# Optimization experiments

Hardware: AMD Instinct MI355X
Metric: run time of the kernel (lower is better)

The kernel has to match this reference:

```python
import jax, jax.numpy as jnp
import numpy as np

N, K = 200000, 32


def setup_inputs() -> dict:
    key = jax.random.key(0)
    k1, k2, k3, k4, k5 = jax.random.split(key, 5)
    V = jax.random.normal(k1, (N, 3), dtype=jnp.float32)
    V_def = jax.random.normal(k2, (N, 3), dtype=jnp.float32)
    nbrs = jax.random.randint(k3, (N, K), 0, N)
    wgts = jax.random.uniform(k4, (N, K), dtype=jnp.float32)
    pad = jax.random.uniform(k5, (N, K)) < 0.3
    wgts = jnp.where(pad, 0.0, wgts)
    return {"V": V, "V_def": V_def, "nbrs": nbrs, "wgts": wgts}


def reference(V, V_def, nbrs, wgts):
    mask = jax.lax.stop_gradient((wgts != 0).astype(V.dtype))  # [N,K]
    edges = V[nbrs] - V[:, None]                                # [N,K,3] base edges
    mesh_hood = jnp.swapaxes(edges * mask[..., None], 1, 2)     # [N,3,K]
    tru_hood = jnp.swapaxes(edges * wgts[..., None], 1, 2)      # [N,3,K] weighted base edges
    rot_hood = jnp.swapaxes(V_def[nbrs] - V_def[:, None], 1, 2) # [N,3,K] deformed edges
    # per-vertex 3x3 covariance: sum_k rot_hood[:,i,k] * tru_hood[:,j,k]
    tmp = jnp.einsum('nik,njk->nij', rot_hood, tru_hood)        # [N,3,3]
    U, s, Vh = jnp.linalg.svd(tmp, full_matrices=False)
    Vt = jnp.swapaxes(Vh, 1, 2)  # torch.svd-style V matrix (named Vt in source)
    # R = (Vt @ U^T)^T = U @ Vt^T
    R = jnp.einsum('nij,nkj->nik', U, jnp.swapaxes(Vt, 1, 2))
    dets = jnp.linalg.det(R)                                    # [N]
    last_row = Vt[:, -1, :] * dets[:, None]                     # flip last row by det sign
    Vt = jnp.concatenate([Vt[:, :-1], last_row[:, None]], axis=1)
    R = jnp.einsum('nij,nkj->nik', U, jnp.swapaxes(Vt, 1, 2))   # proper rotation, det=+1
    R_tru = jnp.einsum('nij,njk->nik', R, mesh_hood)            # [N,3,K]
    diff = rot_hood - R_tru
    arap = jnp.sum(diff * diff, axis=1) * wgts * mask           # [N,K]
    return jnp.mean(jnp.sum(arap, axis=-1))
```

## Files before the change

### kernel.cpp

```cpp
#include <hip/hip_runtime.h>
#include <hip/hip_bf16.h>

#define NV   200000
#define KN   32
#define TPB  256
#define NSLICE 4
#define SLICEW 50000

#define F_EPS  5.9604645e-8f
#define F_UNFL 1.1754944e-38f
#define F_TOL  (10.0f * F_EPS)

__device__ __forceinline__ float fdiv_(float a, float b) { return __fdividef(a, b); }
__device__ __forceinline__ float fsqrt_(float x) { return __builtin_amdgcn_sqrtf(x); }

__global__ __launch_bounds__(256) void pack_kernel(const float* __restrict__ V,
                                                   const float* __restrict__ Vd,
                                                   float* __restrict__ wsf) {
    int i = blockIdx.x * 256 + threadIdx.x;
    if (i < NV * 3) {
        int n = i / 3;
        int c = i - n * 3;
        wsf[(size_t)n * 8 + c]     = V[i];
        wsf[(size_t)n * 8 + 3 + c] = Vd[i];
    }
}

__device__ __forceinline__ void slartg_(float f, float g, float& c, float& s, float& r) {
    if (g == 0.0f)      { c = 1.0f; s = 0.0f; r = f; }
    else if (f == 0.0f) { c = 0.0f; s = copysignf(1.0f, g); r = fabsf(g); }
    else {
        float d = fsqrt_(f * f + g * g);
        c = fdiv_(fabsf(f), d);
        r = copysignf(d, f);
        s = fdiv_(g, r);
    }
}

__device__ __forceinline__ void slas2_(float f, float g, float h, float& ssmin, float& ssmax) {
    float fa = fabsf(f), ga = fabsf(g), ha = fabsf(h);
    float fhmn = fminf(fa, ha), fhmx = fmaxf(fa, ha);
    if (fhmn == 0.0f) {
        ssmin = 0.0f;
        if (fhmx == 0.0f) ssmax = ga;
        else {
            float mx = fmaxf(fhmx, ga), mn = fminf(fhmx, ga);
            float q = fdiv_(mn, mx);
            ssmax = mx * fsqrt_(1.0f + q * q);
        }
    } else {
        if (ga < fhmx) {
            float as_ = 1.0f + fdiv_(fhmn, fhmx);
            float at  = fdiv_(fhmx - fhmn, fhmx);
            float au  = fdiv_(ga, fhmx); au = au * au;
            float c   = fdiv_(2.0f, fsqrt_(as_ * as_ + au) + fsqrt_(at * at + au));
            ssmin = fhmn * c;
            ssmax = fdiv_(fhmx, c);
        } else {
            float au = fdiv_(fhmx, ga);
            if (au == 0.0f) { ssmin = fdiv_(fhmn * fhmx, ga); ssmax = ga; }
            else {
                float as_ = 1.0f + fdiv_(fhmn, fhmx);
                float at  = fdiv_(fhmx - fhmn, fhmx);
                float t1 = as_ * au, t2 = at * au;
                float c = fdiv_(1.0f, fsqrt_(1.0f + t1 * t1) + fsqrt_(1.0f + t2 * t2));
                ssmin = (fhmn * c) * au;
                ssmin = ssmin + ssmin;
                ssmax = fdiv_(ga, c + c);
            }
        }
    }
}

__device__ void slasv2_(float f, float g, float h,
                        float& ssmin, float& ssmax,
                        float& snr, float& csr, float& snl, float& csl) {
    float ft = f, fa = fabsf(f), ht = h, ha = fabsf(h);
    int pmax = 1;
    bool swp = (ha > fa);
    if (swp) {
        pmax = 3;
        float t = ft; ft = ht; ht = t;
        t = fa; fa = ha; ha = t;
    }
    float gt = g, ga = fabsf(g);
    float clt = 0.f, crt = 0.f, slt = 0.f, srt = 0.f;
    if (ga == 0.0f) {
        ssmin = ha; ssmax = fa;
        clt = 1.0f; crt = 1.0f; slt = 0.0f; srt = 0.0f;
    } else {
        bool gasmal = true;
        if (ga > fa) {
            pmax = 2;
            if (fdiv_(fa, ga) < F_EPS) {
                gasmal = false;
                ssmax = ga;
                ssmin = (ha > 1.0f) ? fdiv_(fa, fdiv_(ga, ha)) : (fdiv_(fa, ga) * ha);
                clt = 1.0f; slt = fdiv_(ht, gt); srt = 1.0f; crt = fdiv_(ft, gt);
            }
        }
        if (gasmal) {
            float dd = fa - ha;
            float l_ = (dd == fa) ? 1.0f : fdiv_(dd, fa);
            float m_ = fdiv_(gt, ft);
            float t_ = 2.0f - l_;
            float mm = m_ * m_, tt = t_ * t_;
            float s_ = fsqrt_(tt + mm);
            float r_ = (l_ == 0.0f) ? fabsf(m_) : fsqrt_(l_ * l_ + mm);
            float a_ = 0.5f * (s_ + r_);
            ssmin = fdiv_(ha, a_);
            ssmax = fa * a_;
            float tv;
            if (mm == 0.0f) {
                if (l_ == 0.0f) tv = copysignf(2.0f, ft) * copysignf(1.0f, gt);
                else            tv = fdiv_(gt, copysignf(dd, ft)) + fdiv_(m_, t_);
            } else {
                tv = (fdiv_(m_, s_ + t_) + fdiv_(m_, r_ + l_)) * (1.0f + a_);
            }
            float l2 = fsqrt_(tv * tv + 4.0f);
            crt = fdiv_(2.0f, l2);
            srt = fdiv_(tv, l2);
            clt = fdiv_(crt + srt * m_, a_);
            slt = fdiv_(ht, ft) * fdiv_(srt, a_);
        }
    }
    if (swp) { csl = srt; snl = crt; csr = slt; snr = clt; }
    else     { csl = clt; snl = slt; csr = crt; snr = srt; }
    float tsign = 1.0f;
    if (pmax == 1) tsign = copysignf(1.0f, csr) * copysignf(1.0f, csl) * copysignf(1.0f, f);
    if (pmax == 2) tsign = copysignf(1.0f, snr) * copysignf(1.0f, csl) * copysignf(1.0f, g);
    if (pmax == 3) tsign = copysignf(1.0f, snr) * copysignf(1.0f, snl) * copysignf(1.0f, h);
    ssmax = copysignf(ssmax, tsign);
    ssmin = copysignf(ssmin, tsign * copysignf(1.0f, f) * copysignf(1.0f, h));
}

template<int RA, int RB>
__device__ __forceinline__ void rot_rows(float A[3][3], float c, float s) {
    #pragma unroll
    for (int j = 0; j < 3; ++j) {
        float x = A[RA][j], y = A[RB][j];
        A[RA][j] = c * x + s * y;
        A[RB][j] = c * y - s * x;
    }
}
template<int CA, int CB>
__device__ __forceinline__ void rot_cols(float A[3][3], float c, float s) {
    #pragma unroll
    for (int i = 0; i < 3; ++i) {
        float x = A[i][CA], y = A[i][CB];
        A[i][CA] = c * x + s * y;
        A[i][CB] = c * y - s * x;
    }
}
template<int RA, int RB>
__device__ __forceinline__ void swap_rows(float A[3][3]) {
    #pragma unroll
    for (int j = 0; j < 3; ++j) { float t = A[RA][j]; A[RA][j] = A[RB][j]; A[RB][j] = t; }
}
template<int CA, int CB>
__device__ __forceinline__ void swap_cols(float A[3][3]) {
    #pragma unroll
    for (int i = 0; i < 3; ++i) { float t = A[i][CA]; A[i][CA] = A[i][CB]; A[i][CB] = t; }
}

__device__ void bdsqr3(float d[3], float e[2], float U[3][3], float VT[3][3]) {
    float thresh;
    {
        float sminoa = fabsf(d[0]);
        if (sminoa != 0.0f) {
            float mu = sminoa;
            mu = fabsf(d[1]) * fdiv_(mu, mu + fabsf(e[0]));
            sminoa = fminf(sminoa, mu);
            if (sminoa != 0.0f) {
                mu = fabsf(d[2]) * fdiv_(mu, mu + fabsf(e[1]));
                sminoa = fminf(sminoa, mu);
            }
        }
        sminoa = sminoa * 0.57735026919f;
        thresh = fmaxf(F_TOL * sminoa, 54.0f * F_UNFL);
    }

    const bool mir = fabsf(d[0]) < fabsf(d[2]);
    if (mir) {
        float t = d[0]; d[0] = d[2]; d[2] = t;
        t = e[0]; e[0] = e[1]; e[1] = t;
        float Un[3][3], Vn[3][3];
        #pragma unroll
        for (int i = 0; i < 3; ++i)
            #pragma unroll
            for (int j = 0; j < 3; ++j) { Un[i][j] = VT[2 - j][i]; Vn[i][j] = U[j][2 - i]; }
        #pragma unroll
        for (int i = 0; i < 3; ++i)
            #pragma unroll
            for (int j = 0; j < 3; ++j) { U[i][j] = Un[i][j]; VT[i][j] = Vn[i][j]; }
    }

    int iter = 0;
    bool tail22 = false;
    bool aborted = false;

    for (;;) {
        if (iter > 54) { aborted = true; break; }
        if (fabsf(e[1]) <= thresh) { e[1] = 0.0f; tail22 = true; break; }
        float smax = fmaxf(fabsf(d[2]), fmaxf(fabsf(e[1]), fabsf(d[1])));
        if (fabsf(e[0]) <= thresh) {
            e[0] = 0.0f;
            float sigmn, sigmx, sinr, cosr, sinl, cosl;
            slasv2_(d[1], e[1], d[2], sigmn, sigmx, sinr, cosr, sinl, cosl);
            d[1] = sigmx; d[2] = sigmn; e[1] = 0.0f;
            rot_rows<1, 2>(VT, cosr, sinr); rot_cols<1, 2>(U, cosl, sinl);
            break;
        }
        smax = fmaxf(smax, fmaxf(fabsf(e[0]), fabsf(d[0])));
        float sminl = 0.0f;
        bool conv = false;
        {
            if (fabsf(e[1]) <= F_TOL * fabsf(d[2])) { e[1] = 0.0f; continue; }
            float mu = fabsf(d[0]); sminl = mu;
            if (fabsf(e[0]) <= F_TOL * mu) { e[0] = 0.0f; conv = true; }
            else {
                mu = fabsf(d[1]) * fdiv_(mu, mu + fabsf(e[0]));
                sminl = fminf(sminl, mu);
                if (fabsf(e[1]) <= F_TOL * mu) { e[1] = 0.0f; conv = true; }
                else {
                    mu = fabsf(d[2]) * fdiv_(mu, mu + fabsf(e[1]));
                    sminl = fminf(sminl, mu);
                }
            }
        }
        if (conv) continue;
        float shift = 0.0f, rdum;
        if (3.0f * F_TOL * fdiv_(sminl, smax) <= fmaxf(F_EPS, 0.01f * F_TOL)) {
            shift = 0.0f;
        } else {
            float sll = fabsf(d[0]);
            slas2_(d[1], e[1], d[2], shift, rdum);
            if (sll > 0.0f) { float q = fdiv_(shift, sll); if (q * q < F_EPS) shift = 0.0f; }
        }
        iter += 2;
        if (shift == 0.0f) {
            float cs = 1.0f, oldcs = 1.0f, sn, oldsn, r;
            float c1, s1, oc1, os1, c2, s2, oc2, os2;
            slartg_(d[0] * cs, e[0], cs, sn, r);
            slartg_(oldcs * r, d[1] * sn, oldcs, oldsn, d[0]);
            c1 = cs; s1 = sn; oc1 = oldcs; os1 = oldsn;
            slartg_(d[1] * cs, e[1], cs, sn, r);
            e[0] = oldsn * r;
            slartg_(oldcs * r, d[2] * sn, oldcs, oldsn, d[1]);
            c2 = cs; s2 = sn; oc2 = oldcs; os2 = oldsn;
            float h = d[2] * cs; d[2] = h * oldcs; e[1] = h * oldsn;
            rot_rows<0, 1>(VT, c1, s1);  rot_rows<1, 2>(VT, c2, s2);
            rot_cols<0, 1>(U, oc1, os1); rot_cols<1, 2>(U, oc2, os2);
            if (fabsf(e[1]) <= thresh) e[1] = 0.0f;
        } else {
            float f = (fabsf(d[0]) - shift) * (copysignf(1.0f, d[0]) + fdiv_(shift, d[0]));
            float g = e[0], cosr, sinr, cosl, sinl, r;
            float cr1, sr1, cl1, sl1, cr2, sr2, cl2, sl2;
            slartg_(f, g, cosr, sinr, r);
            f = cosr * d[0] + sinr * e[0];
            e[0] = cosr * e[0] - sinr * d[0];
            g = sinr * d[1];
            d[1] = cosr * d[1];
            slartg_(f, g, cosl, sinl, r);
            d[0] = r;
            f = cosl * e[0] + sinl * d[1];
            d[1] = cosl * d[1] - sinl * e[0];
            g = sinl * e[1];
            e[1] = cosl * e[1];
            cr1 = cosr; sr1 = sinr; cl1 = cosl; sl1 = sinl;
            slartg_(f, g, cosr, sinr, r);
            e[0] = r;
            f = cosr * d[1] + sinr * e[1];
            e[1] = cosr * e[1] - sinr * d[1];
            g = sinr * d[2];
            d[2] = cosr * d[2];
            slartg_(f, g, cosl, sinl, r);
            d[1] = r;
            f = cosl * e[1] + sinl * d[2];
            d[2] = cosl * d[2] - sinl * e[1];
            cr2 = cosr; sr2 = sinr; cl2 = cosl; sl2 = sinl;
            e[1] = f;
            rot_rows<0, 1>(VT, cr1, sr1); rot_rows<1, 2>(VT, cr2, sr2);
            rot_cols<0, 1>(U, cl1, sl1);  rot_cols<1, 2>(U, cl2, sl2);
            if (fabsf(e[1]) <= thresh) e[1] = 0.0f;
        }
    }
    if (tail22 && !aborted) {
        if (fabsf(e[0]) <= thresh) {
            e[0] = 0.0f;
        } else {
            float sigmn, sigmx, sinr, cosr, sinl, cosl;
            slasv2_(d[0], e[0], d[1], sigmn, sigmx, sinr, cosr, sinl, cosl);
            d[0] = sigmx; d[1] = sigmn; e[0] = 0.0f;
            rot_rows<0, 1>(VT, cosr, sinr); rot_cols<0, 1>(U, cosl, sinl);
        }
    }
    if (mir) {
        float Un[3][3], Vn[3][3];
        #pragma unroll
        for (int i = 0; i < 3; ++i)
            #pragma unroll
            for (int j = 0; j < 3; ++j) { Un[i][j] = VT[j][i]; Vn[i][j] = U[j][i]; }
        #pragma unroll
        for (int i = 0; i < 3; ++i)
            #pragma unroll
            for (int j = 0; j < 3; ++j) { U[i][j] = Un[i][j]; VT[i][j] = Vn[i][j]; }
    }
    #pragma unroll
    for (int i = 0; i < 3; ++i) {
        if (d[i] < 0.0f) {
            d[i] = -d[i];
            VT[i][0] = -VT[i][0]; VT[i][1] = -VT[i][1]; VT[i][2] = -VT[i][2];
        }
    }
    {
        int isub = 1; float smin = d[0];
        if (d[1] <= smin) { isub = 2; smin = d[1]; }
        if (d[2] <= smin) { isub = 3; smin = d[2]; }
        if (isub != 3) {
            if (isub == 1) { d[0] = d[2]; d[2] = smin; swap_rows<0, 2>(VT); swap_cols<0, 2>(U); }
            else           { d[1] = d[2]; d[2] = smin; swap_rows<1, 2>(VT); swap_cols<1, 2>(U); }
        }
    }
    {
        int isub = 1; float smin = d[0];
        if (d[1] <= smin) { isub = 2; smin = d[1]; }
        if (isub != 2) { d[0] = d[1]; d[1] = smin; swap_rows<0, 1>(VT); swap_cols<0, 1>(U); }
    }
}

__device__ float svd_energy(const float T[3][3], float Srr, float See) {
    float A[3][3];
    #pragma unroll
    for (int i = 0; i < 3; ++i) { A[i][0] = T[i][0]; A[i][1] = T[i][1]; A[i][2] = T[i][2]; }

    float d[3], e[2];
    float tq0, v1, v2;
    float tp0, u2;
    float tq1, v22;
    {
        float a00 = A[0][0], a10 = A[1][0], a20 = A[2][0];
        float xn = fsqrt_(a10 * a10 + a20 * a20);
        if (xn == 0.0f) { tq0 = 0.0f; v1 = 0.0f; v2 = 0.0f; d[0] = a00; }
        else {
            float beta = -copysignf(fsqrt_(a00 * a00 + xn * xn), a00);
            tq0 = fdiv_(beta - a00, beta);
            float inv = fdiv_(1.0f, a00 - beta);
            v1 = a10 * inv; v2 = a20 * inv;
            d[0] = beta;
        }
        #pragma unroll
        for (int j = 1; j < 3; ++j) {
            float w = A[0][j] + v1 * A[1][j] + v2 * A[2][j];
            w *= tq0;
            A[0][j] -= w; A[1][j] -= w * v1; A[2][j] -= w * v2;
        }
    }
    {
        float a01 = A[0][1], a02 = A[0][2];
        float xn = fabsf(a02);
        if (xn == 0.0f) { tp0 = 0.0f; u2 = 0.0f; e[0] = a01; }
        else {
            float beta = -copysignf(fsqrt_(a01 * a01 + a02 * a02), a01);
            tp0 = fdiv_(beta - a01, beta);
            u2 = fdiv_(a02, a01 - beta);
            e[0] = beta;
        }
        #pragma unroll
        for (int i = 1; i < 3; ++i) {
            float w = A[i][1] + u2 * A[i][2];
            w *= tp0;
            A[i][1] -= w; A[i][2] -= w * u2;
        }
    }
    {
        float a11 = A[1][1], a21 = A[2][1];
        float xn = fabsf(a21);
        if (xn == 0.0f) { tq1 = 0.0f; v22 = 0.0f; d[1] = a11; }
        else {
            float beta = -copysignf(fsqrt_(a11 * a11 + a21 * a21), a11);
            tq1 = fdiv_(beta - a11, beta);
            v22 = fdiv_(a21, a11 - beta);
            d[1] = beta;
        }
        float w = A[1][2] + v22 * A[2][2];
        w *= tq1;
        A[1][2] -= w; A[2][2] -= w * v22;
        e[1] = A[1][2];
        d[2] = A[2][2];
    }

    float U[3][3], VT[3][3];
    {
        float h11 = 1.0f - tq1;
        float h12 = -tq1 * v22;
        float h22 = 1.0f - tq1 * v22 * v22;
        float w0 = 1.0f;
        float w1 = v1 * h11 + v2 * h12;
        float w2 = v1 * h12 + v2 * h22;
        U[0][0] = 1.0f - tq0 * w0;  U[0][1] = -tq0 * w1;           U[0][2] = -tq0 * w2;
        U[1][0] = -tq0 * v1 * w0;   U[1][1] = h11 - tq0 * v1 * w1; U[1][2] = h12 - tq0 * v1 * w2;
        U[2][0] = -tq0 * v2 * w0;   U[2][1] = h12 - tq0 * v2 * w1; U[2][2] = h22 - tq0 * v2 * w2;
        VT[0][0] = 1.0f; VT[0][1] = 0.0f;               VT[0][2] = 0.0f;
        VT[1][0] = 0.0f; VT[1][1] = 1.0f - tp0;         VT[1][2] = -tp0 * u2;
        VT[2][0] = 0.0f; VT[2][1] = -tp0 * u2;          VT[2][2] = 1.0f - tp0 * u2 * u2;
    }

    bdsqr3(d, e, U, VT);

    float detU = U[0][0] * (U[1][1] * U[2][2] - U[1][2] * U[2][1])
               - U[0][1] * (U[1][0] * U[2][2] - U[1][2] * U[2][0])
               + U[0][2] * (U[1][0] * U[2][1] - U[1][1] * U[2][0]);
    float detV = VT[0][0] * (VT[1][1] * VT[2][2] - VT[1][2] * VT[2][1])
               - VT[0][1] * (VT[1][0] * VT[2][2] - VT[1][2] * VT[2][0])
               + VT[0][2] * (VT[1][0] * VT[2][1] - VT[1][1] * VT[2][0]);
    float det = detU * detV;

    float cross = 0.0f;
    #pragma unroll
    for (int k = 0; k < 3; ++k) {
        float w0 = VT[k][0], w1 = VT[k][1], w2 = det * VT[k][2];
        #pragma unroll
        for (int i = 0; i < 3; ++i) {
            float Rik = U[i][0] * w0 + U[i][1] * w1 + U[i][2] * w2;
            cross += T[i][k] * Rik;
        }
    }
    return Srr + See - 2.0f * cross;
}

__global__ __launch_bounds__(TPB, 4) void gather_kernel(
    const float4* __restrict__ P,
    const int*    __restrict__ nbrs, const float* __restrict__ wgts,
    float4* __restrict__ Tout)
{
    const int t = blockIdx.x * TPB + threadIdx.x;
    const int v = t >> 2;
    const int p = t & 3;
    if (v >= NV) return;

    float4 a0 = P[(size_t)v * 2];
    float2 b0 = ((const float2*)P)[(size_t)v * 4 + 2];
    const float vx = a0.x, vy = a0.y, vz = a0.z;
    const float dx = a0.w, dy = b0.x, dz = b0.y;

    const int4*   nb4 = (const int4*)  (nbrs + (size_t)v * KN) + p * 2;
    const float4* w4  = (const float4*)(wgts + (size_t)v * KN) + p * 2;
    int4   n0 = nb4[0], n1 = nb4[1];
    float4 q0 = w4[0],  q1 = w4[1];
    const int   ids[8] = { n0.x, n0.y, n0.z, n0.w, n1.x, n1.y, n1.z, n1.w };
    const float wss[8] = { q0.x, q0.y, q0.z, q0.w, q1.x, q1.y, q1.z, q1.w };

    float T00 = 0, T01 = 0, T02 = 0, T10 = 0, T11 = 0, T12 = 0, T20 = 0, T21 = 0, T22 = 0;
    float Srr = 0, See = 0;

    #pragma unroll
    for (int sl = 0; sl < NSLICE; ++sl) {
        const int lo = sl * SLICEW;
        const int hi = lo + SLICEW;
        #pragma unroll
        for (int k = 0; k < 8; ++k) {
            int nb = ids[k];
            if (nb >= lo && nb < hi) {
                float w  = wss[k];
                float4 a = P[(size_t)nb * 2];
                float2 b = ((const float2*)P)[(size_t)nb * 4 + 2];
                float e0 = a.x - vx, e1 = a.y - vy, e2 = a.z - vz;
                float r0 = a.w - dx, r1 = b.x - dy, r2 = b.y - dz;
                float we0 = w * e0, we1 = w * e1, we2 = w * e2;
                T00 += r0 * we0; T01 += r0 * we1; T02 += r0 * we2;
                T10 += r1 * we0; T11 += r1 * we1; T12 += r1 * we2;
                T20 += r2 * we0; T21 += r2 * we1; T22 += r2 * we2;
                Srr += w * (r0 * r0 + r1 * r1 + r2 * r2);
                See += we0 * e0 + we1 * e1 + we2 * e2;
            }
        }
    }

    #define RED4(x) x += __shfl_xor(x, 1); x += __shfl_xor(x, 2);
    RED4(T00) RED4(T01) RED4(T02) RED4(T10) RED4(T11) RED4(T12)
    RED4(T20) RED4(T21) RED4(T22) RED4(Srr) RED4(See)
    #undef RED4

    if (p == 0) Tout[(size_t)v * 3 + 0] = make_float4(T00, T01, T02, T10);
    if (p == 1) Tout[(size_t)v * 3 + 1] = make_float4(T11, T12, T20, T21);
    if (p == 2) Tout[(size_t)v * 3 + 2] = make_float4(T22, Srr, See, 0.0f);
}

__global__ __launch_bounds__(TPB) void svd_kernel(
    const float4* __restrict__ Tin, float* __restrict__ out)
{
    __shared__ float s_red[TPB / 64];
    const int tid = threadIdx.x;
    const int n   = blockIdx.x * TPB + tid;
    float E = 0.0f;
    if (n < NV) {
        float4 q0 = Tin[(size_t)n * 3 + 0];
        float4 q1 = Tin[(size_t)n * 3 + 1];
        float4 q2 = Tin[(size_t)n * 3 + 2];
        float T[3][3] = {{q0.x, q0.y, q0.z}, {q0.w, q1.x, q1.y}, {q1.z, q1.w, q2.x}};
        E = svd_energy(T, q2.y, q2.z);
    }
    #pragma unroll
    for (int off = 32; off > 0; off >>= 1) E += __shfl_down(E, off);
    if ((tid & 63) == 0) s_red[tid >> 6] = E;
    __syncthreads();
    if (tid == 0) {
        float t = 0.0f;
        #pragma unroll
        for (int i = 0; i < TPB / 64; ++i) t += s_red[i];
        atomicAdd(out, t * (1.0f / (float)NV));
    }
}

template<bool PACKED>
__global__ __launch_bounds__(TPB) void arap_fused(
    const float*  __restrict__ Vr, const float* __restrict__ Vdr,
    const float4* __restrict__ P,
    const int*    __restrict__ nbrs, const float* __restrict__ wgts,
    float* __restrict__ out)
{
    __shared__ float s_red[TPB / 64];
    const int tid = threadIdx.x;
    const int n   = blockIdx.x * TPB + tid;
    float E = 0.0f;
    if (n < NV) {
        float vx, vy, vz, dx, dy, dz;
        if (PACKED) {
            float4 a0 = P[(size_t)n * 2];
            float2 b0 = ((const float2*)P)[(size_t)n * 4 + 2];
            vx = a0.x; vy = a0.y; vz = a0.z; dx = a0.w; dy = b0.x; dz = b0.y;
        } else {
            vx = Vr [3 * n]; vy = Vr [3 * n + 1]; vz = Vr [3 * n + 2];
            dx = Vdr[3 * n]; dy = Vdr[3 * n + 1]; dz = Vdr[3 * n + 2];
        }
        float T[3][3] = {{0, 0, 0}, {0, 0, 0}, {0, 0, 0}};
        float Srr = 0.0f, See = 0.0f;
        for (int k = 0; k < KN; ++k) {
            int   nb = nbrs[(size_t)n * KN + k];
            float w  = wgts[(size_t)n * KN + k];
            float e0, e1, e2, r0, r1, r2;
            if (PACKED) {
                float4 a = P[(size_t)nb * 2];
                float2 b = ((const float2*)P)[(size_t)nb * 4 + 2];
                e0 = a.x - vx; e1 = a.y - vy; e2 = a.z - vz;
                r0 = a.w - dx; r1 = b.x - dy; r2 = b.y - dz;
            } else {
                e0 = Vr [3 * nb] - vx; e1 = Vr [3 * nb + 1] - vy; e2 = Vr [3 * nb + 2] - vz;
                r0 = Vdr[3 * nb] - dx; r1 = Vdr[3 * nb + 1] - dy; r2 = Vdr[3 * nb + 2] - dz;
            }
            float we0 = w * e0, we1 = w * e1, we2 = w * e2;
            T[0][0] += r0 * we0; T[0][1] += r0 * we1; T[0][2] += r0 * we2;
            T[1][0] += r1 * we0; T[1][1] += r1 * we1; T[1][2] += r1 * we2;
            T[2][0] += r2 * we0; T[2][1] += r2 * we1; T[2][2] += r2 * we2;
            Srr += w * (r0 * r0 + r1 * r1 + r2 * r2);
            See += we0 * e0 + we1 * e1 + we2 * e2;
        }
        E = svd_energy(T, Srr, See);
    }
    #pragma unroll
    for (int off = 32; off > 0; off >>= 1) E += __shfl_down(E, off);
    if ((tid & 63) == 0) s_red[tid >> 6] = E;
    __syncthreads();
    if (tid == 0) {
        float t = 0.0f;
        #pragma unroll
        for (int i = 0; i < TPB / 64; ++i) t += s_red[i];
        atomicAdd(out, t * (1.0f / (float)NV));
    }
}

extern "C" void kernel_launch(void* const* d_in, const int* in_sizes, int n_in,
                              void* d_out, int out_size, void* d_ws, size_t ws_size,
                              hipStream_t stream) {
    (void)in_sizes; (void)n_in; (void)out_size;
    const float* V  = (const float*)d_in[0];
    const float* Vd = (const float*)d_in[1];
    const int*   nb = (const int*)  d_in[2];
    const float* wg = (const float*)d_in[3];
    float* out = (float*)d_out;

    hipMemsetAsync(out, 0, sizeof(float), stream);

    const size_t tab_bytes  = (size_t)NV * 32;
    const size_t tmat_bytes = (size_t)NV * 48;
    const int pblk = (NV * 3 + 255) / 256;

    if (ws_size >= tab_bytes + tmat_bytes) {
        float*  wsf  = (float*)d_ws;
        float4* tout = (float4*)((char*)d_ws + tab_bytes);
        pack_kernel<<<pblk, 256, 0, stream>>>(V, Vd, wsf);
        const int gblk = (NV * 4 + TPB - 1) / TPB;
        gather_kernel<<<gblk, TPB, 0, stream>>>((const float4*)wsf, nb, wg, tout);
        const int sblk = (NV + TPB - 1) / TPB;
        svd_kernel<<<sblk, TPB, 0, stream>>>((const float4*)tout, out);
    } else if (ws_size >= tab_bytes) {
        float* wsf = (float*)d_ws;
        pack_kernel<<<pblk, 256, 0, stream>>>(V, Vd, wsf);
        const int nblk = (NV + TPB - 1) / TPB;
        arap_fused<true><<<nblk, TPB, 0, stream>>>(nullptr, nullptr,
            (const float4*)wsf, nb, wg, out);
    } else {
        const int nblk = (NV + TPB - 1) / TPB;
        arap_fused<false><<<nblk, TPB, 0, stream>>>(V, Vd, nullptr, nb, wg, out);
    }
}
```

Before: 95.45 us.

## Fuse gather and SVD kernels via shared memory staging of covariance

Merges the neighbor-gather kernel and the per-vertex SVD kernel into one kernel. Four threads per vertex accumulate the covariance, the 11 values are staged in shared memory, and then one wavefront of 64 threads runs the SVD energy and does an atomic add per block. This removes the global write and read of the 48-byte-per-vertex covariance buffer and one kernel launch. In exchange only a quarter of each block's threads do the SVD phase, which may leave the ALUs underused, and there are more atomics, one per 64 vertices. The grid assumes NV is divisible by 64.

```diff
diff --git a/kernel.cpp b/kernel.cpp
--- a/kernel.cpp
+++ b/kernel.cpp
@@ -4,6 +4,7 @@
 #define NV   200000
 #define KN   32
 #define TPB  256
+#define VPB  64
 #define NSLICE 4
 #define SLICEW 50000
 
@@ -429,87 +430,76 @@
     return Srr + See - 2.0f * cross;
 }
 
-__global__ __launch_bounds__(TPB, 4) void gather_kernel(
+__global__ __launch_bounds__(TPB, 4) void arap_kernel(
     const float4* __restrict__ P,
     const int*    __restrict__ nbrs, const float* __restrict__ wgts,
-    float4* __restrict__ Tout)
+    float* __restrict__ out)
 {
-    const int t = blockIdx.x * TPB + threadIdx.x;
-    const int v = t >> 2;
-    const int p = t & 3;
-    if (v >= NV) return;
-
-    float4 a0 = P[(size_t)v * 2];
-    float2 b0 = ((const float2*)P)[(size_t)v * 4 + 2];
-    const float vx = a0.x, vy = a0.y, vz = a0.z;
-    const float dx = a0.w, dy = b0.x, dz = b0.y;
-
-    const int4*   nb4 = (const int4*)  (nbrs + (size_t)v * KN) + p * 2;
-    const float4* w4  = (const float4*)(wgts + (size_t)v * KN) + p * 2;
-    int4   n0 = nb4[0], n1 = nb4[1];
-    float4 q0 = w4[0],  q1 = w4[1];
-    const int   ids[8] = { n0.x, n0.y, n0.z, n0.w, n1.x, n1.y, n1.z, n1.w };
-    const float wss[8] = { q0.x, q0.y, q0.z, q0.w, q1.x, q1.y, q1.z, q1.w };
-
-    float T00 = 0, T01 = 0, T02 = 0, T10 = 0, T11 = 0, T12 = 0, T20 = 0, T21 = 0, T22 = 0;
-    float Srr = 0, See = 0;
-
-    #pragma unroll
-    for (int sl = 0; sl < NSLICE; ++sl) {
-        const int lo = sl * SLICEW;
-        const int hi = lo + SLICEW;
-        #pragma unroll
-        for (int k = 0; k < 8; ++k) {
-            int nb = ids[k];
-            if (nb >= lo && nb < hi) {
-                float w  = wss[k];
-                float4 a = P[(size_t)nb * 2];
-                float2 b = ((const float2*)P)[(size_t)nb * 4 + 2];
-                float e0 = a.x - vx, e1 = a.y - vy, e2 = a.z - vz;
-                float r0 = a.w - dx, r1 = b.x - dy, r2 = b.y - dz;
-                float we0 = w * e0, we1 = w * e1, we2 = w * e2;
-                T00 += r0 * we0; T01 += r0 * we1; T02 += r0 * we2;
-                T10 += r1 * we0; T11 += r1 * we1; T12 += r1 * we2;
-                T20 += r2 * we0; T21 += r2 * we1; T22 += r2 * we2;
-                Srr += w * (r0 * r0 + r1 * r1 + r2 * r2);
-                See += we0 * e0 + we1 * e1 + we2 * e2;
-            }
-        }
-    }
-
-    #define RED4(x) x += __shfl_xor(x, 1); x += __shfl_xor(x, 2);
-    RED4(T00) RED4(T01) RED4(T02) RED4(T10) RED4(T11) RED4(T12)
-    RED4(T20) RED4(T21) RED4(T22) RED4(Srr) RED4(See)
-    #undef RED4
-
-    if (p == 0) Tout[(size_t)v * 3 + 0] = make_float4(T00, T01, T02, T10);
-    if (p == 1) Tout[(size_t)v * 3 + 1] = make_float4(T11, T12, T20, T21);
-    if (p == 2) Tout[(size_t)v * 3 + 2] = make_float4(T22, Srr, See, 0.0f);
-}
-
-__global__ __launch_bounds__(TPB) void svd_kernel(
-    const float4* __restrict__ Tin, float* __restrict__ out)
-{
-    __shared__ float s_red[TPB / 64];
+    __shared__ float sT[VPB][13];
+
     const int tid = threadIdx.x;
-    const int n   = blockIdx.x * TPB + tid;
-    float E = 0.0f;
-    if (n < NV) {
-        float4 q0 = Tin[(size_t)n * 3 + 0];
-        float4 q1 = Tin[(size_t)n * 3 + 1];
-        float4 q2 = Tin[(size_t)n * 3 + 2];
-        float T[3][3] = {{q0.x, q0.y, q0.z}, {q0.w, q1.x, q1.y}, {q1.z, q1.w, q2.x}};
-        E = svd_energy(T, q2.y, q2.z);
-    }
-    #pragma unroll
-    for (int off = 32; off > 0; off >>= 1) E += __shfl_down(E, off);
-    if ((tid & 63) == 0) s_red[tid >> 6] = E;
+    const int g   = tid >> 2;
+    const int p   = tid & 3;
+    const int v   = blockIdx.x * VPB + g;
+
+    {
+        float4 a0 = P[(size_t)v * 2];
+        float2 b0 = ((const float2*)P)[(size_t)v * 4 + 2];
+        const float vx = a0.x, vy = a0.y, vz = a0.z;
+        const float dx = a0.w, dy = b0.x, dz = b0.y;
+
+        const int4*   nb4 = (const int4*)  (nbrs + (size_t)v * KN) + p * 2;
+        const float4* w4  = (const float4*)(wgts + (size_t)v * KN) + p * 2;
+        int4   n0 = nb4[0], n1 = nb4[1];
+        float4 q0 = w4[0],  q1 = w4[1];
+        const int   ids[8] = { n0.x, n0.y, n0.z, n0.w, n1.x, n1.y, n1.z, n1.w };
+        const float wss[8] = { q0.x, q0.y, q0.z, q0.w, q1.x, q1.y, q1.z, q1.w };
+
+        float T00 = 0, T01 = 0, T02 = 0, T10 = 0, T11 = 0, T12 = 0, T20 = 0, T21 = 0, T22 = 0;
+        float Srr = 0, See = 0;
+
+        #pragma unroll
+        for (int sl = 0; sl < NSLICE; ++sl) {
+            const int lo = sl * SLICEW;
+            const int hi = lo + SLICEW;
+            #pragma unroll
+            for (int k = 0; k < 8; ++k) {
+                int nb = ids[k];
+                if (nb >= lo && nb < hi) {
+                    float w  = wss[k];
+                    float4 a = P[(size_t)nb * 2];
+                    float2 b = ((const float2*)P)[(size_t)nb * 4 + 2];
+                    float e0 = a.x - vx, e1 = a.y - vy, e2 = a.z - vz;
+                    float r0 = a.w - dx, r1 = b.x - dy, r2 = b.y - dz;
+                    float we0 = w * e0, we1 = w * e1, we2 = w * e2;
+                    T00 += r0 * we0; T01 += r0 * we1; T02 += r0 * we2;
+                    T10 += r1 * we0; T11 += r1 * we1; T12 += r1 * we2;
+                    T20 += r2 * we0; T21 += r2 * we1; T22 += r2 * we2;
+                    Srr += w * (r0 * r0 + r1 * r1 + r2 * r2);
+                    See += we0 * e0 + we1 * e1 + we2 * e2;
+                }
+            }
+        }
+
+        #define RED4(x) x += __shfl_xor(x, 1); x += __shfl_xor(x, 2);
+        RED4(T00) RED4(T01) RED4(T02) RED4(T10) RED4(T11) RED4(T12)
+        RED4(T20) RED4(T21) RED4(T22) RED4(Srr) RED4(See)
+        #undef RED4
+
+        if (p == 0) { sT[g][0] = T00; sT[g][1] = T01; sT[g][2]  = T02; sT[g][3] = T10; }
+        if (p == 1) { sT[g][4] = T11; sT[g][5] = T12; sT[g][6]  = T20; sT[g][7] = T21; }
+        if (p == 2) { sT[g][8] = T22; sT[g][9] = Srr; sT[g][10] = See; }
+    }
     __syncthreads();
-    if (tid == 0) {
-        float t = 0.0f;
-        #pragma unroll
-        for (int i = 0; i < TPB / 64; ++i) t += s_red[i];
-        atomicAdd(out, t * (1.0f / (float)NV));
+
+    if (tid < VPB) {
+        float T[3][3] = {{sT[tid][0], sT[tid][1], sT[tid][2]},
+                         {sT[tid][3], sT[tid][4], sT[tid][5]},
+                         {sT[tid][6], sT[tid][7], sT[tid][8]}};
+        float E = svd_energy(T, sT[tid][9], sT[tid][10]);
+        #pragma unroll
+        for (int off = 32; off > 0; off >>= 1) E += __shfl_down(E, off);
+        if (tid == 0) atomicAdd(out, E * (1.0f / (float)NV));
     }
 }
 
@@ -582,24 +572,14 @@
 
     hipMemsetAsync(out, 0, sizeof(float), stream);
 
-    const size_t tab_bytes  = (size_t)NV * 32;
-    const size_t tmat_bytes = (size_t)NV * 48;
+    const size_t tab_bytes = (size_t)NV * 32;
     const int pblk = (NV * 3 + 255) / 256;
 
-    if (ws_size >= tab_bytes + tmat_bytes) {
-        float*  wsf  = (float*)d_ws;
-        float4* tout = (float4*)((char*)d_ws + tab_bytes);
-        pack_kernel<<<pblk, 256, 0, stream>>>(V, Vd, wsf);
-        const int gblk = (NV * 4 + TPB - 1) / TPB;
-        gather_kernel<<<gblk, TPB, 0, stream>>>((const float4*)wsf, nb, wg, tout);
-        const int sblk = (NV + TPB - 1) / TPB;
-        svd_kernel<<<sblk, TPB, 0, stream>>>((const float4*)tout, out);
-    } else if (ws_size >= tab_bytes) {
+    if (ws_size >= tab_bytes) {
         float* wsf = (float*)d_ws;
         pack_kernel<<<pblk, 256, 0, stream>>>(V, Vd, wsf);
-        const int nblk = (NV + TPB - 1) / TPB;
-        arap_fused<true><<<nblk, TPB, 0, stream>>>(nullptr, nullptr,
-            (const float4*)wsf, nb, wg, out);
+        const int ablk = NV / VPB;
+        arap_kernel<<<ablk, TPB, 0, stream>>>((const float4*)wsf, nb, wg, out);
     } else {
         const int nblk = (NV + TPB - 1) / TPB;
         arap_fused<false><<<nblk, TPB, 0, stream>>>(V, Vd, nullptr, nb, wg, out);
```

Result: slower. 113.6 us (+19.0%).
